# Optimization experiments

Measured on AMD Instinct MI355X. Metric: run time of the kernel, lower is better.

Reference implementation:

```python
import jax, jax.numpy as jnp
import numpy as np

C = 256
DQK = 32  # in_dim // factor

def setup_inputs() -> dict:
    key = jax.random.key(0)
    ks = jax.random.split(key, 8)
    B, H, W = 4, 64, 64
    x = jax.random.normal(ks[0], (B, C, H, W), dtype=jnp.float32)
    s = 1.0 / np.sqrt(C)
    Wq = jax.random.normal(ks[1], (DQK, C), dtype=jnp.float32) * s
    bq = jnp.zeros((DQK,), dtype=jnp.float32)
    Wk = jax.random.normal(ks[2], (DQK, C), dtype=jnp.float32) * s
    bk = jnp.zeros((DQK,), dtype=jnp.float32)
    Wv = jax.random.normal(ks[3], (C, C), dtype=jnp.float32) * s
    bv = jnp.zeros((C,), dtype=jnp.float32)
    # torch inits gamma to 0 (which would zero most grads); use a nonzero scalar
    gamma = jnp.array([0.5], dtype=jnp.float32)
    return {"x": x, "Wq": Wq, "bq": bq, "Wk": Wk, "bk": bk,
            "Wv": Wv, "bv": bv, "gamma": gamma}

def reference(x, Wq, bq, Wk, bk, Wv, bv, gamma):
    B, Cc, H, W = x.shape
    N = H * W
    def conv1x1(w, b):
        return jnp.einsum('bchw,oc->bohw', x, w) + b[None, :, None, None]
    q = conv1x1(Wq, bq).reshape(B, -1, N)   # [B, dqk, N]
    k = conv1x1(Wk, bk).reshape(B, -1, N)   # [B, dqk, N]
    energy = jnp.einsum('bdn,bdm->bnm', q, k)          # [B, N, N]
    attention = jax.nn.softmax(energy, axis=-1)
    v = conv1x1(Wv, bv).reshape(B, Cc, N)   # [B, C, N]
    # out = bmm(v, attention^T): out[b,c,n] = sum_m v[b,c,m] * attn[b,n,m]
    out = jnp.einsum('bcm,bnm->bcn', v, attention).reshape(B, Cc, H, W)
    weighted_out = gamma[0] * out
    final = weighted_out + x
    return (final, weighted_out, attention)
```

## Files before the change

### kernel.cpp

```cpp
#include <hip/hip_runtime.h>
#include <stdint.h>

#define CC 256
#define NNq 4096

typedef float f32x4 __attribute__((ext_vector_type(4)));
typedef short bf16x8 __attribute__((ext_vector_type(8)));

#define MFMA16(a, b, c) __builtin_amdgcn_mfma_f32_16x16x32_bf16(a, b, c, 0, 0, 0)

static __device__ __forceinline__ short f2bf(float f) {
  unsigned u = __builtin_bit_cast(unsigned, f);
  u += 0x7fffu + ((u >> 16) & 1u);
  return (short)(u >> 16);
}
static __device__ __forceinline__ float bf2f(short s) {
  return __builtin_bit_cast(float, ((unsigned)(unsigned short)s) << 16);
}

#define SBAR() do { \
  __builtin_amdgcn_sched_barrier(0); \
  asm volatile("s_waitcnt lgkmcnt(0)" ::: "memory"); \
  __builtin_amdgcn_s_barrier(); \
  __builtin_amdgcn_sched_barrier(0); \
} while (0)

#define XSTR 66

__global__ __launch_bounds__(256) void proj_kernel(
    const float* __restrict__ x,
    const float* __restrict__ Wq, const float* __restrict__ bq,
    const float* __restrict__ Wk, const float* __restrict__ bk,
    const float* __restrict__ Wv, const float* __restrict__ bv,
    unsigned short* __restrict__ qh_, unsigned short* __restrict__ ql_,
    unsigned short* __restrict__ kh_, unsigned short* __restrict__ kl_,
    unsigned short* __restrict__ v5)
{
  __shared__ float xs[256 * XSTR];
  const int t = threadIdx.x;
  const int b = blockIdx.x >> 6;
  const int n0 = (blockIdx.x & 63) << 6;
  const float L2E = 1.4426950408889634f;

  const float* xb = x + ((size_t)b * CC) * NNq + n0;
#pragma unroll
  for (int i = 0; i < 16; ++i) {
    int fi = i * 256 + t;
    int c = fi >> 4, nv = (fi & 15) << 2;
    float4 v4 = *(const float4*)(xb + (size_t)c * NNq + nv);
    float* d = &xs[c * XSTR + nv];
    d[0] = v4.x; d[1] = v4.y; d[2] = v4.z; d[3] = v4.w;
  }
  __syncthreads();

  const int w = t >> 6, l = t & 63;
  const int l15 = l & 15, l4 = l >> 4;

  f32x4 acc[5][4];
#pragma unroll
  for (int r5 = 0; r5 < 5; ++r5) {
    int rt = w * 5 + r5;
    const float* bias; float bscale;
    if (rt < 16)      { bias = bv + rt * 16;        bscale = 1.f; }
    else if (rt < 18) { bias = bq + (rt - 16) * 16; bscale = L2E; }
    else              { bias = bk + (rt - 18) * 16; bscale = 1.f; }
#pragma unroll
    for (int j = 0; j < 4; ++j) {
      float bval = bias[l4 * 4 + j] * bscale;
#pragma unroll
      for (int nt = 0; nt < 4; ++nt) acc[r5][nt][j] = bval;
    }
  }

#pragma unroll 1
  for (int ks = 0; ks < 8; ++ks) {
    bf16x8 ah[5], al[5];
#pragma unroll
    for (int r5 = 0; r5 < 5; ++r5) {
      int rt = w * 5 + r5;
      const float* wrow; float wscale;
      if (rt < 16)      { wrow = Wv + (size_t)(rt * 16 + l15) * 256;        wscale = 1.f; }
      else if (rt < 18) { wrow = Wq + (size_t)((rt - 16) * 16 + l15) * 256; wscale = L2E; }
      else              { wrow = Wk + (size_t)((rt - 18) * 16 + l15) * 256; wscale = 1.f; }
      const float* src = wrow + ks * 32 + l4 * 8;
#pragma unroll
      for (int i = 0; i < 8; ++i) {
        float v = src[i] * wscale;
        short hh = f2bf(v);
        ah[r5][i] = hh;
        al[r5][i] = f2bf(v - bf2f(hh));
      }
    }
#pragma unroll
    for (int nt = 0; nt < 4; ++nt) {
      bf16x8 bh, bl;
#pragma unroll
      for (int i = 0; i < 8; ++i) {
        float v = xs[(ks * 32 + l4 * 8 + i) * XSTR + nt * 16 + l15];
        short hh = f2bf(v);
        bh[i] = hh;
        bl[i] = f2bf(v - bf2f(hh));
      }
#pragma unroll
      for (int r5 = 0; r5 < 5; ++r5) {
        acc[r5][nt] = MFMA16(ah[r5], bl, acc[r5][nt]);
        acc[r5][nt] = MFMA16(al[r5], bh, acc[r5][nt]);
        acc[r5][nt] = MFMA16(ah[r5], bh, acc[r5][nt]);
      }
    }
  }

#pragma unroll
  for (int r5 = 0; r5 < 5; ++r5) {
    int rt = w * 5 + r5;
#pragma unroll
    for (int nt = 0; nt < 4; ++nt) {
      int n = n0 + nt * 16 + l15;
#pragma unroll
      for (int j = 0; j < 4; ++j) {
        float v = acc[r5][nt][j];
        int sub = l4 * 4 + j;
        if (rt < 16) {
          int c = rt * 16 + sub;
          size_t o = (((size_t)b * 128 + (n >> 5)) * 256 + c) * 32 + (n & 31);
          v5[o] = (unsigned short)f2bf(v);
        } else {
          short hh = f2bf(v);
          short lo = f2bf(v - bf2f(hh));
          unsigned short* dh = (rt < 18) ? qh_ : kh_;
          unsigned short* dl = (rt < 18) ? ql_ : kl_;
          int d = ((rt < 18) ? (rt - 16) : (rt - 18)) * 16 + sub;
          size_t o = ((size_t)b * NNq + n) * 32 + d;
          dh[o] = (unsigned short)hh;
          dl[o] = (unsigned short)lo;
        }
      }
    }
  }
}

__global__ __launch_bounds__(512, 4) void attn_pv_kernel(
    const unsigned short* __restrict__ qh_, const unsigned short* __restrict__ ql_,
    const unsigned short* __restrict__ kh_, const unsigned short* __restrict__ kl_,
    const unsigned short* __restrict__ v5, const float* __restrict__ x,
    const float* __restrict__ gamma, float* __restrict__ out)
{
  __shared__ __align__(16) unsigned short p_lds[2][4096];
  __shared__ float sums_lds[8][32];

  const int t = threadIdx.x, w = t >> 6, l = t & 63;
  const int l15 = l & 15, l4 = l >> 4;
  const int sb = ((blockIdx.x & 7) << 6) | (blockIdx.x >> 3);
  const int b = sb >> 7;
  const int n0 = (sb & 127) << 5;
  const int g = w >> 2, h = w & 3;
  const int h32 = h * 32;

  const unsigned short* khb = kh_ + (size_t)b * NNq * 32;
  const unsigned short* klb = kl_ + (size_t)b * NNq * 32;
  const unsigned short* vbb = v5 + (size_t)b * 1048576;
  float* attn = out + 8388608 + (size_t)b * NNq * NNq + (size_t)n0 * NNq;

  bf16x8 q2h[2], q2l[2];
#pragma unroll
  for (int rg = 0; rg < 2; ++rg) {
    size_t qo = ((size_t)b * NNq + n0 + rg * 16 + l15) * 32 + l4 * 8;
    q2h[rg] = *(const bf16x8*)(qh_ + qo);
    q2l[rg] = *(const bf16x8*)(ql_ + qo);
  }

  float sx[2][4] = {{0.f,0.f,0.f,0.f},{0.f,0.f,0.f,0.f}};
  {
    const int mq = w * 512;
    bf16x8 kch[2], kcl[2];
#pragma unroll
    for (int mt = 0; mt < 2; ++mt) {
      size_t ko = (size_t)(mq + mt * 16 + l15) * 32 + l4 * 8;
      kch[mt] = *(const bf16x8*)(khb + ko);
      kcl[mt] = *(const bf16x8*)(klb + ko);
    }
#pragma unroll 1
    for (int it = 0; it < 16; ++it) {
      const int nx = mq + ((it + 1) & 15) * 32;
      bf16x8 knh[2], knl[2];
#pragma unroll
      for (int mt = 0; mt < 2; ++mt) {
        size_t ko = (size_t)(nx + mt * 16 + l15) * 32 + l4 * 8;
        knh[mt] = *(const bf16x8*)(khb + ko);
        knl[mt] = *(const bf16x8*)(klb + ko);
      }
#pragma unroll
      for (int mt = 0; mt < 2; ++mt) {
#pragma unroll
        for (int rg = 0; rg < 2; ++rg) {
          f32x4 e = {0.f, 0.f, 0.f, 0.f};
          e = MFMA16(q2h[rg], kcl[mt], e);
          e = MFMA16(q2l[rg], kch[mt], e);
          e = MFMA16(q2h[rg], kch[mt], e);
#pragma unroll
          for (int j = 0; j < 4; ++j) sx[rg][j] += exp2f(e[j] - 64.0f);
        }
      }
      kch[0] = knh[0]; kch[1] = knh[1];
      kcl[0] = knl[0]; kcl[1] = knl[1];
    }
  }
#pragma unroll
  for (int mask = 1; mask < 16; mask <<= 1)
#pragma unroll
    for (int rg = 0; rg < 2; ++rg)
#pragma unroll
      for (int j = 0; j < 4; ++j) sx[rg][j] += __shfl_xor(sx[rg][j], mask);
  if (l15 == 0) {
#pragma unroll
    for (int rg = 0; rg < 2; ++rg)
#pragma unroll
      for (int j = 0; j < 4; ++j)
        sums_lds[w][rg * 16 + l4 * 4 + j] = sx[rg][j];
  }
  __syncthreads();
  const bf16x8 qh = q2h[g], qlo = q2l[g];
  f32x4 crow;
#pragma unroll
  for (int j = 0; j < 4; ++j) {
    int r = g * 16 + l4 * 4 + j;
    float S = 0.f;
#pragma unroll
    for (int ww = 0; ww < 8; ++ww) S += sums_lds[ww][r];
    crow[j] = 64.0f + log2f(S);
  }

  f32x4 acc[2][2];
#pragma unroll
  for (int ct = 0; ct < 2; ++ct)
#pragma unroll
    for (int nt = 0; nt < 2; ++nt) acc[ct][nt] = f32x4{0.f, 0.f, 0.f, 0.f};

  bf16x8 pw;

  auto loadK = [&](int chunk, bf16x8 (&KH)[2], bf16x8 (&KL)[2]) {
#pragma unroll
    for (int sub = 0; sub < 2; ++sub) {
      size_t ko = (size_t)(chunk * 128 + h32 + sub * 16 + l15) * 32 + l4 * 8;
      KH[sub] = *(const bf16x8*)(khb + ko);
      KL[sub] = *(const bf16x8*)(klb + ko);
    }
  };
  auto estep = [&](int ec, const bf16x8 (&KH)[2], const bf16x8 (&KL)[2]) {
    const int mbE = ec * 128;
#pragma unroll
    for (int sub = 0; sub < 2; ++sub) {
      f32x4 e = {0.f, 0.f, 0.f, 0.f};
      e = MFMA16(qh, KL[sub], e);
      e = MFMA16(qlo, KH[sub], e);
      e = MFMA16(qh, KH[sub], e);
#pragma unroll
      for (int j = 0; j < 4; ++j) {
        float p = exp2f(e[j] - crow[j]);
        int nl = g * 16 + l4 * 4 + j;
        int ml = h32 + sub * 16 + l15;
        __builtin_nontemporal_store(p, attn + (size_t)nl * NNq + mbE + ml);
        pw[sub * 4 + j] = f2bf(p);
      }
    }
  };
  auto pwrite = [&](int par) {
    char* pld = (char*)p_lds[par];
#pragma unroll
    for (int sub = 0; sub < 2; ++sub)
#pragma unroll
      for (int j = 0; j < 4; ++j) {
        int nl = g * 16 + l4 * 4 + j;
        int ml = h32 + sub * 16 + l15;
        int byteo = nl * 256 + ((ml * 2) ^ ((nl & 7) << 4));
        *(unsigned short*)(pld + byteo) = (unsigned short)pw[sub * 4 + j];
      }
  };

  bf16x8 kAh[2], kAl[2];
  loadK(0, kAh, kAl);
  estep(0, kAh, kAl);
  pwrite(0);
  loadK(1, kAh, kAl);

#pragma unroll 1
  for (int it = 0; it < 32; ++it) {
    bf16x8 vfA[2][2], vfB[2][2];
#pragma unroll
    for (int ct = 0; ct < 2; ++ct)
#pragma unroll
      for (int ms = 0; ms < 2; ++ms) {
        size_t vo = (size_t)(it * 4 + ms) * 8192 +
                    (size_t)(w * 32 + ct * 16 + l15) * 32 + l4 * 8;
        vfA[ct][ms] = *(const bf16x8*)(vbb + vo);
      }
    bf16x8 kBh[2], kBl[2];
    loadK((it + 2) & 31, kBh, kBl);
    if (it < 31) estep(it + 1, kAh, kAl);
#pragma unroll
    for (int ct = 0; ct < 2; ++ct)
#pragma unroll
      for (int ms = 2; ms < 4; ++ms) {
        size_t vo = (size_t)(it * 4 + ms) * 8192 +
                    (size_t)(w * 32 + ct * 16 + l15) * 32 + l4 * 8;
        vfB[ct][ms - 2] = *(const bf16x8*)(vbb + vo);
      }
    SBAR();
    if (it < 31) pwrite((it + 1) & 1);
    char* pl = (char*)p_lds[it & 1];
    __builtin_amdgcn_s_setprio(1);
#pragma unroll
    for (int ms = 0; ms < 4; ++ms) {
      int mbyte = ms * 64 + l4 * 16;
      int o0 = l15 * 256 + (mbyte ^ ((l15 & 7) << 4));
      int o1 = (16 + l15) * 256 + (mbyte ^ (((16 + l15) & 7) << 4));
      bf16x8 pf0 = *(const bf16x8*)(pl + o0);
      bf16x8 pf1 = *(const bf16x8*)(pl + o1);
#pragma unroll
      for (int ct = 0; ct < 2; ++ct) {
        bf16x8 vv = (ms < 2) ? vfA[ct][ms & 1] : vfB[ct][ms & 1];
        acc[ct][0] = MFMA16(vv, pf0, acc[ct][0]);
        acc[ct][1] = MFMA16(vv, pf1, acc[ct][1]);
      }
    }
    __builtin_amdgcn_s_setprio(0);
#pragma unroll
    for (int sub = 0; sub < 2; ++sub) { kAh[sub] = kBh[sub]; kAl[sub] = kBl[sub]; }
  }

  const float gm = gamma[0];
#pragma unroll
  for (int ct = 0; ct < 2; ++ct) {
#pragma unroll
    for (int nt = 0; nt < 2; ++nt) {
#pragma unroll
      for (int j = 0; j < 4; ++j) {
        int c = w * 32 + ct * 16 + l4 * 4 + j;
        int n = n0 + nt * 16 + l15;
        size_t go = ((size_t)b * CC + c) * NNq + n;
        float o = acc[ct][nt][j] * gm;
        out[4194304 + go] = o;
        out[go] = o + x[go];
      }
    }
  }
}

extern "C" void kernel_launch(void* const* d_in, const int* in_sizes, int n_in,
                              void* d_out, int out_size, void* d_ws, size_t ws_size,
                              hipStream_t stream) {
  const float* x     = (const float*)d_in[0];
  const float* Wq    = (const float*)d_in[1];
  const float* bq    = (const float*)d_in[2];
  const float* Wk    = (const float*)d_in[3];
  const float* bk    = (const float*)d_in[4];
  const float* Wv    = (const float*)d_in[5];
  const float* bv    = (const float*)d_in[6];
  const float* gamma = (const float*)d_in[7];
  float* out = (float*)d_out;

  char* ws = (char*)d_ws;
  unsigned short* qh   = (unsigned short*)(ws);
  unsigned short* ql   = (unsigned short*)(ws + (1u << 20));
  unsigned short* kh   = (unsigned short*)(ws + (2u << 20));
  unsigned short* kl   = (unsigned short*)(ws + (3u << 20));
  unsigned short* v5   = (unsigned short*)(ws + (4u << 20));

  proj_kernel<<<256, 256, 0, stream>>>(x, Wq, bq, Wk, bk, Wv, bv, qh, ql, kh, kl, v5);
  attn_pv_kernel<<<512, 512, 0, stream>>>(qh, ql, kh, kl, v5, x, gamma, out);
}
```

Before: 163.5 us.

## Split attention into unnormalized PV kernel and separate attention-write kernel

The fused kernel used to run a separate pass computing softmax row sums before the PV loop, then wrote the normalized attention matrix inside the PV loop. Now the PV kernel accumulates unnormalized exp values and their row sums in a single pass, normalizing the output at the end. It stores per-row log-sums to the workspace. A new kernel then recomputes the energies and writes the normalized attention with vectorized nontemporal stores. This removes the extra sum pass and the scattered scalar stores from the PV kernel, at the cost of a third launch and recomputing QK. The PV product now uses bf16 probabilities computed against a fixed offset instead of the true max, which changes rounding behavior.

```diff
diff --git a/kernel.cpp b/kernel.cpp
--- a/kernel.cpp
+++ b/kernel.cpp
@@ -139,11 +139,12 @@
   }
 }
 
-__global__ __launch_bounds__(512, 4) void attn_pv_kernel(
+__global__ __launch_bounds__(512, 4) void pv_kernel(
     const unsigned short* __restrict__ qh_, const unsigned short* __restrict__ ql_,
     const unsigned short* __restrict__ kh_, const unsigned short* __restrict__ kl_,
     const unsigned short* __restrict__ v5, const float* __restrict__ x,
-    const float* __restrict__ gamma, float* __restrict__ out)
+    const float* __restrict__ gamma, float* __restrict__ Crow,
+    float* __restrict__ out)
 {
   __shared__ __align__(16) unsigned short p_lds[2][4096];
   __shared__ float sums_lds[8][32];
@@ -159,76 +160,10 @@
   const unsigned short* khb = kh_ + (size_t)b * NNq * 32;
   const unsigned short* klb = kl_ + (size_t)b * NNq * 32;
   const unsigned short* vbb = v5 + (size_t)b * 1048576;
-  float* attn = out + 8388608 + (size_t)b * NNq * NNq + (size_t)n0 * NNq;
-
-  bf16x8 q2h[2], q2l[2];
-#pragma unroll
-  for (int rg = 0; rg < 2; ++rg) {
-    size_t qo = ((size_t)b * NNq + n0 + rg * 16 + l15) * 32 + l4 * 8;
-    q2h[rg] = *(const bf16x8*)(qh_ + qo);
-    q2l[rg] = *(const bf16x8*)(ql_ + qo);
-  }
-
-  float sx[2][4] = {{0.f,0.f,0.f,0.f},{0.f,0.f,0.f,0.f}};
-  {
-    const int mq = w * 512;
-    bf16x8 kch[2], kcl[2];
-#pragma unroll
-    for (int mt = 0; mt < 2; ++mt) {
-      size_t ko = (size_t)(mq + mt * 16 + l15) * 32 + l4 * 8;
-      kch[mt] = *(const bf16x8*)(khb + ko);
-      kcl[mt] = *(const bf16x8*)(klb + ko);
-    }
-#pragma unroll 1
-    for (int it = 0; it < 16; ++it) {
-      const int nx = mq + ((it + 1) & 15) * 32;
-      bf16x8 knh[2], knl[2];
-#pragma unroll
-      for (int mt = 0; mt < 2; ++mt) {
-        size_t ko = (size_t)(nx + mt * 16 + l15) * 32 + l4 * 8;
-        knh[mt] = *(const bf16x8*)(khb + ko);
-        knl[mt] = *(const bf16x8*)(klb + ko);
-      }
-#pragma unroll
-      for (int mt = 0; mt < 2; ++mt) {
-#pragma unroll
-        for (int rg = 0; rg < 2; ++rg) {
-          f32x4 e = {0.f, 0.f, 0.f, 0.f};
-          e = MFMA16(q2h[rg], kcl[mt], e);
-          e = MFMA16(q2l[rg], kch[mt], e);
-          e = MFMA16(q2h[rg], kch[mt], e);
-#pragma unroll
-          for (int j = 0; j < 4; ++j) sx[rg][j] += exp2f(e[j] - 64.0f);
-        }
-      }
-      kch[0] = knh[0]; kch[1] = knh[1];
-      kcl[0] = knl[0]; kcl[1] = knl[1];
-    }
-  }
-#pragma unroll
-  for (int mask = 1; mask < 16; mask <<= 1)
-#pragma unroll
-    for (int rg = 0; rg < 2; ++rg)
-#pragma unroll
-      for (int j = 0; j < 4; ++j) sx[rg][j] += __shfl_xor(sx[rg][j], mask);
-  if (l15 == 0) {
-#pragma unroll
-    for (int rg = 0; rg < 2; ++rg)
-#pragma unroll
-      for (int j = 0; j < 4; ++j)
-        sums_lds[w][rg * 16 + l4 * 4 + j] = sx[rg][j];
-  }
-  __syncthreads();
-  const bf16x8 qh = q2h[g], qlo = q2l[g];
-  f32x4 crow;
-#pragma unroll
-  for (int j = 0; j < 4; ++j) {
-    int r = g * 16 + l4 * 4 + j;
-    float S = 0.f;
-#pragma unroll
-    for (int ww = 0; ww < 8; ++ww) S += sums_lds[ww][r];
-    crow[j] = 64.0f + log2f(S);
-  }
+
+  const size_t qbase = ((size_t)b * NNq + n0 + g * 16 + l15) * 32 + l4 * 8;
+  const bf16x8 qh = *(const bf16x8*)(qh_ + qbase);
+  const bf16x8 qlo = *(const bf16x8*)(ql_ + qbase);
 
   f32x4 acc[2][2];
 #pragma unroll
@@ -236,6 +171,7 @@
 #pragma unroll
     for (int nt = 0; nt < 2; ++nt) acc[ct][nt] = f32x4{0.f, 0.f, 0.f, 0.f};
 
+  float sx[4] = {0.f, 0.f, 0.f, 0.f};
   bf16x8 pw;
 
   auto loadK = [&](int chunk, bf16x8 (&KH)[2], bf16x8 (&KL)[2]) {
@@ -246,8 +182,7 @@
       KL[sub] = *(const bf16x8*)(klb + ko);
     }
   };
-  auto estep = [&](int ec, const bf16x8 (&KH)[2], const bf16x8 (&KL)[2]) {
-    const int mbE = ec * 128;
+  auto estep = [&](const bf16x8 (&KH)[2], const bf16x8 (&KL)[2]) {
 #pragma unroll
     for (int sub = 0; sub < 2; ++sub) {
       f32x4 e = {0.f, 0.f, 0.f, 0.f};
@@ -256,10 +191,8 @@
       e = MFMA16(qh, KH[sub], e);
 #pragma unroll
       for (int j = 0; j < 4; ++j) {
-        float p = exp2f(e[j] - crow[j]);
-        int nl = g * 16 + l4 * 4 + j;
-        int ml = h32 + sub * 16 + l15;
-        __builtin_nontemporal_store(p, attn + (size_t)nl * NNq + mbE + ml);
+        float p = exp2f(e[j] - 64.0f);
+        sx[j] += p;
         pw[sub * 4 + j] = f2bf(p);
       }
     }
@@ -279,7 +212,7 @@
 
   bf16x8 kAh[2], kAl[2];
   loadK(0, kAh, kAl);
-  estep(0, kAh, kAl);
+  estep(kAh, kAl);
   pwrite(0);
   loadK(1, kAh, kAl);
 
@@ -296,7 +229,7 @@
       }
     bf16x8 kBh[2], kBl[2];
     loadK((it + 2) & 31, kBh, kBl);
-    if (it < 31) estep(it + 1, kAh, kAl);
+    if (it < 31) estep(kAh, kAl);
 #pragma unroll
     for (int ct = 0; ct < 2; ++ct)
 #pragma unroll
@@ -328,6 +261,30 @@
     for (int sub = 0; sub < 2; ++sub) { kAh[sub] = kBh[sub]; kAl[sub] = kBl[sub]; }
   }
 
+#pragma unroll
+  for (int mask = 1; mask < 16; mask <<= 1)
+#pragma unroll
+    for (int j = 0; j < 4; ++j) sx[j] += __shfl_xor(sx[j], mask);
+  if (l15 == 0) {
+#pragma unroll
+    for (int j = 0; j < 4; ++j) sums_lds[w][g * 16 + l4 * 4 + j] = sx[j];
+  }
+  __syncthreads();
+
+  float Sinv[2], Sv[2];
+#pragma unroll
+  for (int nt = 0; nt < 2; ++nt) {
+    int r = nt * 16 + l15;
+    float S = sums_lds[nt * 4 + 0][r] + sums_lds[nt * 4 + 1][r] +
+              sums_lds[nt * 4 + 2][r] + sums_lds[nt * 4 + 3][r];
+    Sv[nt] = S;
+    Sinv[nt] = 1.0f / S;
+  }
+  if (w == 0 && l4 == 0) {
+    Crow[(size_t)b * NNq + n0 + l15]      = 64.0f + log2f(Sv[0]);
+    Crow[(size_t)b * NNq + n0 + 16 + l15] = 64.0f + log2f(Sv[1]);
+  }
+
   const float gm = gamma[0];
 #pragma unroll
   for (int ct = 0; ct < 2; ++ct) {
@@ -338,11 +295,66 @@
         int c = w * 32 + ct * 16 + l4 * 4 + j;
         int n = n0 + nt * 16 + l15;
         size_t go = ((size_t)b * CC + c) * NNq + n;
-        float o = acc[ct][nt][j] * gm;
+        float o = acc[ct][nt][j] * Sinv[nt] * gm;
         out[4194304 + go] = o;
         out[go] = o + x[go];
       }
     }
+  }
+}
+
+__global__ __launch_bounds__(256, 4) void attn_write_kernel(
+    const unsigned short* __restrict__ qh_, const unsigned short* __restrict__ ql_,
+    const unsigned short* __restrict__ kh_, const unsigned short* __restrict__ kl_,
+    const float* __restrict__ Crow, float* __restrict__ out)
+{
+  const int t = threadIdx.x, w = t >> 6, l = t & 63;
+  const int l15 = l & 15, l4 = l >> 4;
+  const int sb = ((blockIdx.x & 7) << 7) | (blockIdx.x >> 3);
+  const int b = sb >> 8;
+  const int n0 = (sb & 255) << 4;
+
+  const size_t qbase = ((size_t)b * NNq + n0 + l15) * 32 + l4 * 8;
+  const bf16x8 qbh = *(const bf16x8*)(qh_ + qbase);
+  const bf16x8 qbl = *(const bf16x8*)(ql_ + qbase);
+  const float crn = Crow[(size_t)b * NNq + n0 + l15];
+  const unsigned short* khb = kh_ + (size_t)b * NNq * 32;
+  const unsigned short* klb = kl_ + (size_t)b * NNq * 32;
+  float* arow = out + 8388608 + (size_t)b * NNq * NNq + (size_t)(n0 + l15) * NNq;
+  const int m0 = w * 1024;
+
+  bf16x8 kAh[2], kAl[2];
+#pragma unroll
+  for (int sub = 0; sub < 2; ++sub) {
+    size_t ko = (size_t)(m0 + sub * 16 + l15) * 32 + l4 * 8;
+    kAh[sub] = *(const bf16x8*)(khb + ko);
+    kAl[sub] = *(const bf16x8*)(klb + ko);
+  }
+
+#pragma unroll 1
+  for (int it = 0; it < 32; ++it) {
+    const int mb = m0 + it * 32;
+    const int nx = m0 + ((it + 1) & 31) * 32;
+    bf16x8 kBh[2], kBl[2];
+#pragma unroll
+    for (int sub = 0; sub < 2; ++sub) {
+      size_t ko = (size_t)(nx + sub * 16 + l15) * 32 + l4 * 8;
+      kBh[sub] = *(const bf16x8*)(khb + ko);
+      kBl[sub] = *(const bf16x8*)(klb + ko);
+    }
+#pragma unroll
+    for (int sub = 0; sub < 2; ++sub) {
+      f32x4 e = {0.f, 0.f, 0.f, 0.f};
+      e = MFMA16(kAh[sub], qbl, e);
+      e = MFMA16(kAl[sub], qbh, e);
+      e = MFMA16(kAh[sub], qbh, e);
+      f32x4 p;
+#pragma unroll
+      for (int j = 0; j < 4; ++j) p[j] = exp2f(e[j] - crn);
+      __builtin_nontemporal_store(p, (f32x4*)(arow + mb + sub * 16 + l4 * 4));
+    }
+#pragma unroll
+    for (int sub = 0; sub < 2; ++sub) { kAh[sub] = kBh[sub]; kAl[sub] = kBl[sub]; }
   }
 }
 
@@ -365,7 +377,9 @@
   unsigned short* kh   = (unsigned short*)(ws + (2u << 20));
   unsigned short* kl   = (unsigned short*)(ws + (3u << 20));
   unsigned short* v5   = (unsigned short*)(ws + (4u << 20));
+  float* Crow          = (float*)(ws + (12u << 20));
 
   proj_kernel<<<256, 256, 0, stream>>>(x, Wq, bq, Wk, bk, Wv, bv, qh, ql, kh, kl, v5);
-  attn_pv_kernel<<<512, 512, 0, stream>>>(qh, ql, kh, kl, v5, x, gamma, out);
-}
+  pv_kernel<<<512, 512, 0, stream>>>(qh, ql, kh, kl, v5, x, gamma, Crow, out);
+  attn_write_kernel<<<1024, 256, 0, stream>>>(qh, ql, kh, kl, Crow, out);
+}
```

Result: slower. 215.2 us (+31.6%).

## Specialize warps into producer (energy/softmax) and consumer (PV matmul) groups

Applied to the files above, without the earlier changes.

Splits the 8 waves of the attention+PV kernel into two roles. Waves 0-3 compute the energy tiles, write the attention output and fill the P tile in LDS, and waves 4-7 load V and run the PV MFMAs over 64 channels each. The two groups stay in step through the shared barrier per iteration. This aims to overlap the exp and store-heavy attention work with the matmul work, at the cost of uneven per-wave load and more registers per wave (larger V fragment and accumulator arrays in consumers, more K fragments in producers).

```diff
diff --git a/kernel.cpp b/kernel.cpp
--- a/kernel.cpp
+++ b/kernel.cpp
@@ -153,8 +153,6 @@
   const int sb = ((blockIdx.x & 7) << 6) | (blockIdx.x >> 3);
   const int b = sb >> 7;
   const int n0 = (sb & 127) << 5;
-  const int g = w >> 2, h = w & 3;
-  const int h32 = h * 32;
 
   const unsigned short* khb = kh_ + (size_t)b * NNq * 32;
   const unsigned short* klb = kl_ + (size_t)b * NNq * 32;
@@ -219,128 +217,134 @@
         sums_lds[w][rg * 16 + l4 * 4 + j] = sx[rg][j];
   }
   __syncthreads();
-  const bf16x8 qh = q2h[g], qlo = q2l[g];
-  f32x4 crow;
-#pragma unroll
-  for (int j = 0; j < 4; ++j) {
-    int r = g * 16 + l4 * 4 + j;
-    float S = 0.f;
-#pragma unroll
-    for (int ww = 0; ww < 8; ++ww) S += sums_lds[ww][r];
-    crow[j] = 64.0f + log2f(S);
-  }
-
-  f32x4 acc[2][2];
-#pragma unroll
-  for (int ct = 0; ct < 2; ++ct)
-#pragma unroll
-    for (int nt = 0; nt < 2; ++nt) acc[ct][nt] = f32x4{0.f, 0.f, 0.f, 0.f};
-
-  bf16x8 pw;
-
-  auto loadK = [&](int chunk, bf16x8 (&KH)[2], bf16x8 (&KL)[2]) {
-#pragma unroll
-    for (int sub = 0; sub < 2; ++sub) {
-      size_t ko = (size_t)(chunk * 128 + h32 + sub * 16 + l15) * 32 + l4 * 8;
-      KH[sub] = *(const bf16x8*)(khb + ko);
-      KL[sub] = *(const bf16x8*)(klb + ko);
-    }
-  };
-  auto estep = [&](int ec, const bf16x8 (&KH)[2], const bf16x8 (&KL)[2]) {
-    const int mbE = ec * 128;
-#pragma unroll
-    for (int sub = 0; sub < 2; ++sub) {
-      f32x4 e = {0.f, 0.f, 0.f, 0.f};
-      e = MFMA16(qh, KL[sub], e);
-      e = MFMA16(qlo, KH[sub], e);
-      e = MFMA16(qh, KH[sub], e);
-#pragma unroll
-      for (int j = 0; j < 4; ++j) {
-        float p = exp2f(e[j] - crow[j]);
-        int nl = g * 16 + l4 * 4 + j;
-        int ml = h32 + sub * 16 + l15;
-        __builtin_nontemporal_store(p, attn + (size_t)nl * NNq + mbE + ml);
-        pw[sub * 4 + j] = f2bf(p);
-      }
-    }
-  };
-  auto pwrite = [&](int par) {
-    char* pld = (char*)p_lds[par];
-#pragma unroll
-    for (int sub = 0; sub < 2; ++sub)
-#pragma unroll
-      for (int j = 0; j < 4; ++j) {
-        int nl = g * 16 + l4 * 4 + j;
-        int ml = h32 + sub * 16 + l15;
-        int byteo = nl * 256 + ((ml * 2) ^ ((nl & 7) << 4));
-        *(unsigned short*)(pld + byteo) = (unsigned short)pw[sub * 4 + j];
-      }
-  };
-
-  bf16x8 kAh[2], kAl[2];
-  loadK(0, kAh, kAl);
-  estep(0, kAh, kAl);
-  pwrite(0);
-  loadK(1, kAh, kAl);
+
+  if (w < 4) {
+    const int g = w >> 1, h = w & 1;
+    const bf16x8 qh = q2h[g], qlo = q2l[g];
+    f32x4 crow;
+#pragma unroll
+    for (int j = 0; j < 4; ++j) {
+      int r = g * 16 + l4 * 4 + j;
+      float S = 0.f;
+#pragma unroll
+      for (int ww = 0; ww < 8; ++ww) S += sums_lds[ww][r];
+      crow[j] = 64.0f + log2f(S);
+    }
+
+    bf16x8 kAh[4], kAl[4];
+    bf16x8 pwv[2];
+
+    auto loadK = [&](int chunk, bf16x8 (&KH)[4], bf16x8 (&KL)[4]) {
+#pragma unroll
+      for (int sub = 0; sub < 4; ++sub) {
+        size_t ko = (size_t)(chunk * 128 + h * 64 + sub * 16 + l15) * 32 + l4 * 8;
+        KH[sub] = *(const bf16x8*)(khb + ko);
+        KL[sub] = *(const bf16x8*)(klb + ko);
+      }
+    };
+    auto estep = [&](int ec, const bf16x8 (&KH)[4], const bf16x8 (&KL)[4]) {
+#pragma unroll
+      for (int sub = 0; sub < 4; ++sub) {
+        f32x4 e = {0.f, 0.f, 0.f, 0.f};
+        e = MFMA16(qh, KL[sub], e);
+        e = MFMA16(qlo, KH[sub], e);
+        e = MFMA16(qh, KH[sub], e);
+#pragma unroll
+        for (int j = 0; j < 4; ++j) {
+          float p = exp2f(e[j] - crow[j]);
+          int nl = g * 16 + l4 * 4 + j;
+          int ml = h * 64 + sub * 16 + l15;
+          __builtin_nontemporal_store(p, attn + (size_t)nl * NNq + ec * 128 + ml);
+          pwv[sub >> 1][(sub & 1) * 4 + j] = f2bf(p);
+        }
+      }
+    };
+    auto pwrite = [&](int par) {
+      char* pld = (char*)p_lds[par];
+#pragma unroll
+      for (int sub = 0; sub < 4; ++sub)
+#pragma unroll
+        for (int j = 0; j < 4; ++j) {
+          int nl = g * 16 + l4 * 4 + j;
+          int ml = h * 64 + sub * 16 + l15;
+          int byteo = nl * 256 + ((ml * 2) ^ ((nl & 7) << 4));
+          *(unsigned short*)(pld + byteo) =
+              (unsigned short)pwv[sub >> 1][(sub & 1) * 4 + j];
+        }
+    };
+
+    loadK(0, kAh, kAl);
+    estep(0, kAh, kAl);
+    pwrite(0);
+    loadK(1, kAh, kAl);
 
 #pragma unroll 1
-  for (int it = 0; it < 32; ++it) {
-    bf16x8 vfA[2][2], vfB[2][2];
-#pragma unroll
-    for (int ct = 0; ct < 2; ++ct)
-#pragma unroll
-      for (int ms = 0; ms < 2; ++ms) {
-        size_t vo = (size_t)(it * 4 + ms) * 8192 +
-                    (size_t)(w * 32 + ct * 16 + l15) * 32 + l4 * 8;
-        vfA[ct][ms] = *(const bf16x8*)(vbb + vo);
-      }
-    bf16x8 kBh[2], kBl[2];
-    loadK((it + 2) & 31, kBh, kBl);
-    if (it < 31) estep(it + 1, kAh, kAl);
-#pragma unroll
-    for (int ct = 0; ct < 2; ++ct)
-#pragma unroll
-      for (int ms = 2; ms < 4; ++ms) {
-        size_t vo = (size_t)(it * 4 + ms) * 8192 +
-                    (size_t)(w * 32 + ct * 16 + l15) * 32 + l4 * 8;
-        vfB[ct][ms - 2] = *(const bf16x8*)(vbb + vo);
-      }
-    SBAR();
-    if (it < 31) pwrite((it + 1) & 1);
-    char* pl = (char*)p_lds[it & 1];
-    __builtin_amdgcn_s_setprio(1);
-#pragma unroll
-    for (int ms = 0; ms < 4; ++ms) {
-      int mbyte = ms * 64 + l4 * 16;
-      int o0 = l15 * 256 + (mbyte ^ ((l15 & 7) << 4));
-      int o1 = (16 + l15) * 256 + (mbyte ^ (((16 + l15) & 7) << 4));
-      bf16x8 pf0 = *(const bf16x8*)(pl + o0);
-      bf16x8 pf1 = *(const bf16x8*)(pl + o1);
-#pragma unroll
-      for (int ct = 0; ct < 2; ++ct) {
-        bf16x8 vv = (ms < 2) ? vfA[ct][ms & 1] : vfB[ct][ms & 1];
-        acc[ct][0] = MFMA16(vv, pf0, acc[ct][0]);
-        acc[ct][1] = MFMA16(vv, pf1, acc[ct][1]);
-      }
-    }
-    __builtin_amdgcn_s_setprio(0);
-#pragma unroll
-    for (int sub = 0; sub < 2; ++sub) { kAh[sub] = kBh[sub]; kAl[sub] = kBl[sub]; }
-  }
-
-  const float gm = gamma[0];
-#pragma unroll
-  for (int ct = 0; ct < 2; ++ct) {
-#pragma unroll
-    for (int nt = 0; nt < 2; ++nt) {
-#pragma unroll
-      for (int j = 0; j < 4; ++j) {
-        int c = w * 32 + ct * 16 + l4 * 4 + j;
-        int n = n0 + nt * 16 + l15;
-        size_t go = ((size_t)b * CC + c) * NNq + n;
-        float o = acc[ct][nt][j] * gm;
-        out[4194304 + go] = o;
-        out[go] = o + x[go];
+    for (int it = 0; it < 32; ++it) {
+      bf16x8 kBh[4], kBl[4];
+      loadK((it + 2) & 31, kBh, kBl);
+      if (it < 31) estep(it + 1, kAh, kAl);
+      SBAR();
+      if (it < 31) pwrite((it + 1) & 1);
+#pragma unroll
+      for (int sub = 0; sub < 4; ++sub) { kAh[sub] = kBh[sub]; kAl[sub] = kBl[sub]; }
+    }
+  } else {
+    const int cw = w - 4;
+    f32x4 acc[4][2];
+#pragma unroll
+    for (int ct = 0; ct < 4; ++ct)
+#pragma unroll
+      for (int nt = 0; nt < 2; ++nt) acc[ct][nt] = f32x4{0.f, 0.f, 0.f, 0.f};
+
+    bf16x8 vf[4][4];
+    auto vload = [&](int chunk) {
+#pragma unroll
+      for (int ct = 0; ct < 4; ++ct)
+#pragma unroll
+        for (int ms = 0; ms < 4; ++ms) {
+          size_t vo = (size_t)(chunk * 4 + ms) * 8192 +
+                      (size_t)(cw * 64 + ct * 16 + l15) * 32 + l4 * 8;
+          vf[ct][ms] = *(const bf16x8*)(vbb + vo);
+        }
+    };
+    vload(0);
+
+#pragma unroll 1
+    for (int it = 0; it < 32; ++it) {
+      SBAR();
+      char* pl = (char*)p_lds[it & 1];
+      __builtin_amdgcn_s_setprio(1);
+#pragma unroll
+      for (int ms = 0; ms < 4; ++ms) {
+        int mbyte = ms * 64 + l4 * 16;
+        int o0 = l15 * 256 + (mbyte ^ ((l15 & 7) << 4));
+        int o1 = (16 + l15) * 256 + (mbyte ^ (((16 + l15) & 7) << 4));
+        bf16x8 pf0 = *(const bf16x8*)(pl + o0);
+        bf16x8 pf1 = *(const bf16x8*)(pl + o1);
+#pragma unroll
+        for (int ct = 0; ct < 4; ++ct) {
+          acc[ct][0] = MFMA16(vf[ct][ms], pf0, acc[ct][0]);
+          acc[ct][1] = MFMA16(vf[ct][ms], pf1, acc[ct][1]);
+        }
+      }
+      __builtin_amdgcn_s_setprio(0);
+      if (it < 31) vload(it + 1);
+    }
+
+    const float gm = gamma[0];
+#pragma unroll
+    for (int ct = 0; ct < 4; ++ct) {
+#pragma unroll
+      for (int nt = 0; nt < 2; ++nt) {
+#pragma unroll
+        for (int j = 0; j < 4; ++j) {
+          int c = cw * 64 + ct * 16 + l4 * 4 + j;
+          int n = n0 + nt * 16 + l15;
+          size_t go = ((size_t)b * CC + c) * NNq + n;
+          float o = acc[ct][nt][j] * gm;
+          out[4194304 + go] = o;
+          out[go] = o + x[go];
+        }
       }
     }
   }
```

New measurement: 151.9 us. -7.1%, faster.
